# Kernel tuning notes

Measured on AMD Instinct MI355X. Metric: run time of the kernel, lower is better.

## Reference

```python
import jax, jax.numpy as jnp
import numpy as np

DELTA_A, DELTA_R = 0.1, 1.0
ALPHA, BETA, GAMMA = 1.0, 1.0, 0.001


def setup_inputs() -> dict:
    key = jax.random.key(0)
    B, D, H, W, K = 4, 32, 512, 512, 16
    out = jax.random.normal(key, (B, D, H, W), dtype=jnp.float32)
    # 4x4 block partition -> K=16 instance labels, one center per block
    gh, gw = 4, 4
    bh, bw = H // gh, W // gw
    rows = np.arange(H) // bh  # [H]
    cols = np.arange(W) // bw  # [W]
    labels = (rows[:, None] * gw + cols[None, :]).astype(np.int32)  # [H,W]
    target = jnp.asarray(np.broadcast_to(labels, (B, H, W)).copy())
    ctr = np.array([[r * bh + bh // 2, c * bw + bw // 2]
                    for r in range(gh) for c in range(gw)], dtype=np.int32)  # [K,2]
    centers = jnp.asarray(np.broadcast_to(ctr, (B, K, 2)).copy())
    return {"out": out, "target": target, "centers": centers, "batch_size": B}


def _safe_sqrt(x):
    # matches torch.linalg.norm subgradient 0 at 0 (avoids NaN grads)
    pos = x > 0
    return jnp.where(pos, jnp.sqrt(jnp.where(pos, x, 1.0)), 0.0)


def _pairwise_norm(a, b):
    # a [M,D], b [N,D] -> [M,N] euclidean distances via gram trick
    d2 = (jnp.sum(a * a, 1)[:, None] + jnp.sum(b * b, 1)[None, :]
          - 2.0 * a @ b.T)
    return _safe_sqrt(jax.nn.relu(d2))


def _per_image(o, t, c):
    # o [D,H,W], t [H,W] int, c [K,2] int
    D = o.shape[0]
    K = c.shape[0]
    x = o.reshape(D, -1).T                      # [HW, D]
    E = o[:, c[:, 0], c[:, 1]].T                # [K, D] center embeddings
    lab_c = t[c[:, 0], c[:, 1]]                 # [K]
    mask = (t.reshape(-1)[None, :] == lab_c[:, None])  # [K, HW]
    # attraction: hinged distance of every cluster pixel to its center
    norms = _pairwise_norm(E, x)                # [K, HW]
    hinged = jax.nn.relu(norms - DELTA_A) * mask
    cnt = jnp.sum(mask, axis=1)
    denom = jnp.maximum(cnt - 1, 1).astype(o.dtype)
    s_att = jnp.sum(jnp.sum(hinged, axis=1) / denom)
    # repelling: pairwise center distances; diagonal contributes relu(delta_r)
    # per row and the original subtracts delta_r per center -> excluded
    nE = _pairwise_norm(E, E)                   # [K, K]
    s_rep = jnp.sum(jax.nn.relu(DELTA_R - nE)) - K * DELTA_R
    # regularization: norm of each center embedding
    s_reg = jnp.sum(_safe_sqrt(jnp.sum(E * E, axis=1)))
    return s_att, s_rep, s_reg


def reference(out, target, centers, batch_size):
    K = centers.shape[1]
    s_att, s_rep, s_reg = jax.vmap(_per_image)(out, target, centers)  # [B] each
    div_att = jnp.float32(K)
    div_rep = jnp.float32(K * (K - 1))
    div_reg = jnp.float32(K)

    def step(carry, s):
        a, r, g = carry
        sa, sr, sg = s
        return ((a + sa) / div_att, (r + sr) / div_rep, (g + sg) / div_reg), None

    zero = jnp.float32(0.0)
    (att, rep, reg), _ = jax.lax.scan(step, (zero, zero, zero),
                                      (s_att, s_rep, s_reg))
    loss = ALPHA * att + BETA * rep + GAMMA * reg
    return loss, att, rep
```

## Files before the change

### kernel.cpp

```cpp
#include <hip/hip_runtime.h>
#include <hip/hip_bf16.h>

#define B_ 4
#define D_ 32
#define H_ 512
#define W_ 512
#define K_ 16
#define N_ (H_ * W_)
#define NQ_ (N_ / 4)
#define PADK 17
#define EPAD 33

#define WS_SUM  0
#define WS_CNT  64
#define WS_E2   128
#define WS_LAB  192
#define WS_E    264

__global__ __launch_bounds__(64) void setup_kernel(
    const float* __restrict__ outp, const int* __restrict__ target,
    const int* __restrict__ centers, float* __restrict__ ws) {
  const int b = blockIdx.x, k = blockIdx.y;
  const int lane = threadIdx.x;
  const int cy = centers[(b * K_ + k) * 2 + 0];
  const int cx = centers[(b * K_ + k) * 2 + 1];
  float v = 0.0f;
  if (lane < D_) {
    v = outp[(((size_t)b * D_ + lane) * H_ + cy) * W_ + cx];
    ws[WS_E + (b * K_ + k) * D_ + lane] = v;
  }
  float s = v * v;
  for (int off = 32; off > 0; off >>= 1) s += __shfl_xor(s, off, 64);
  if (lane == 0) {
    ws[WS_E2 + b * K_ + k] = s;
    ((int*)ws)[WS_LAB + b * K_ + k] = target[(size_t)b * N_ + cy * W_ + cx];
    ws[WS_SUM + b * K_ + k] = 0.0f;
    ws[WS_CNT + b * K_ + k] = 0.0f;
  }
}

__global__ __launch_bounds__(256) void attract_kernel(
    const float* __restrict__ outp, const int* __restrict__ target,
    float* __restrict__ ws) {
  const int b = blockIdx.y;
  const int tid = threadIdx.x;
  __shared__ float sE[K_ * EPAD];
  __shared__ float se2[K_];
  __shared__ int slab[K_];
  __shared__ float sacc[256 * PADK];
  __shared__ float scnt[256 * PADK];

  for (int i = tid; i < K_ * D_; i += 256) {
    const int k = i >> 5, d = i & 31;
    sE[k * EPAD + d] = ws[WS_E + b * (K_ * D_) + i];
  }
  if (tid < K_) {
    se2[tid] = ws[WS_E2 + b * K_ + tid];
    slab[tid] = ((const int*)ws)[WS_LAB + b * K_ + tid];
  }
#pragma unroll
  for (int k = 0; k < K_; ++k) {
    sacc[tid * PADK + k] = 0.0f;
    scnt[tid * PADK + k] = 0.0f;
  }
  __syncthreads();

  const int q = blockIdx.x * 256 + tid;
  const float4* xb4 = (const float4*)(outp + (size_t)b * D_ * N_);
  const int4 lab4 = ((const int4*)(target + (size_t)b * N_))[q];
  const int labv[4] = {lab4.x, lab4.y, lab4.z, lab4.w};

  int kf[4], nm[4];
#pragma unroll
  for (int j = 0; j < 4; ++j) {
    kf[j] = 0; nm[j] = 0;
#pragma unroll
    for (int k = 0; k < K_; ++k) {
      if (labv[j] == slab[k]) { if (nm[j] == 0) kf[j] = k; nm[j]++; }
    }
  }

  float dot[4] = {0.f, 0.f, 0.f, 0.f};
  float x2[4] = {0.f, 0.f, 0.f, 0.f};
#pragma unroll 8
  for (int d = 0; d < D_; ++d) {
    const float4 x = xb4[(size_t)d * NQ_ + q];
    const float xs[4] = {x.x, x.y, x.z, x.w};
#pragma unroll
    for (int j = 0; j < 4; ++j) {
      const float e = sE[kf[j] * EPAD + d];
      dot[j] = fmaf(xs[j], e, dot[j]);
      x2[j] = fmaf(xs[j], xs[j], x2[j]);
    }
  }

#pragma unroll
  for (int j = 0; j < 4; ++j) {
    if (nm[j] > 0) {
      const int k = kf[j];
      const float d2 = x2[j] + se2[k] - 2.0f * dot[j];
      const float h = fmaxf(sqrtf(fmaxf(d2, 0.0f)) - 0.1f, 0.0f);
      sacc[tid * PADK + k] += h;
      scnt[tid * PADK + k] += 1.0f;
    }
  }

  const bool extra = (nm[0] > 1) | (nm[1] > 1) | (nm[2] > 1) | (nm[3] > 1);
  if (__any(extra)) {
    for (int k = 0; k < K_; ++k) {
      bool need[4]; bool anyn = false;
#pragma unroll
      for (int j = 0; j < 4; ++j) {
        need[j] = (nm[j] > 1) && (labv[j] == slab[k]) && (k != kf[j]);
        anyn |= need[j];
      }
      if (__any(anyn)) {
        float dt[4] = {0.f, 0.f, 0.f, 0.f};
        for (int d = 0; d < D_; ++d) {
          const float4 x = xb4[(size_t)d * NQ_ + q];
          const float xs[4] = {x.x, x.y, x.z, x.w};
#pragma unroll
          for (int j = 0; j < 4; ++j)
            if (need[j]) dt[j] = fmaf(xs[j], sE[k * EPAD + d], dt[j]);
        }
#pragma unroll
        for (int j = 0; j < 4; ++j) {
          if (need[j]) {
            const float d2 = x2[j] + se2[k] - 2.0f * dt[j];
            const float h = fmaxf(sqrtf(fmaxf(d2, 0.0f)) - 0.1f, 0.0f);
            sacc[tid * PADK + k] += h;
            scnt[tid * PADK + k] += 1.0f;
          }
        }
      }
    }
  }
  __syncthreads();

  const int r = tid >> 4, kk = tid & 15;
  float hsum = 0.0f, csum = 0.0f;
#pragma unroll
  for (int j = 0; j < 16; ++j) {
    hsum += sacc[(r * 16 + j) * PADK + kk];
    csum += scnt[(r * 16 + j) * PADK + kk];
  }
  __syncthreads();
  sacc[r * PADK + kk] = hsum;
  scnt[r * PADK + kk] = csum;
  __syncthreads();
  if (tid < K_) {
    float h = 0.0f, c = 0.0f;
#pragma unroll
    for (int rr = 0; rr < 16; ++rr) {
      h += sacc[rr * PADK + tid];
      c += scnt[rr * PADK + tid];
    }
    atomicAdd(&ws[WS_SUM + b * K_ + tid], h);
    atomicAdd(&ws[WS_CNT + b * K_ + tid], c);
  }
}

__global__ __launch_bounds__(256) void final_kernel(const float* __restrict__ ws,
                                                    float* __restrict__ out) {
  __shared__ float sE[B_ * K_ * D_];
  __shared__ float sred[256];
  __shared__ float srep[B_];
  __shared__ float sreg[B_];
  const int tid = threadIdx.x;
  for (int i = tid; i < B_ * K_ * D_; i += 256) sE[i] = ws[WS_E + i];
  __syncthreads();

  const int i = tid >> 4, j = tid & 15;
  for (int b = 0; b < B_; ++b) {
    float dotv = 0.0f;
    for (int d = 0; d < D_; ++d)
      dotv = fmaf(sE[(b * K_ + i) * D_ + d], sE[(b * K_ + j) * D_ + d], dotv);
    const float d2 = ws[WS_E2 + b * K_ + i] + ws[WS_E2 + b * K_ + j] - 2.0f * dotv;
    sred[tid] = fmaxf(1.0f - sqrtf(fmaxf(d2, 0.0f)), 0.0f);
    __syncthreads();
    for (int s = 128; s > 0; s >>= 1) {
      if (tid < s) sred[tid] += sred[tid + s];
      __syncthreads();
    }
    if (tid == 0) srep[b] = sred[0] - (float)K_;
    __syncthreads();
  }

  sred[tid] = (tid < B_ * K_) ? sqrtf(fmaxf(ws[WS_E2 + tid], 0.0f)) : 0.0f;
  __syncthreads();
  if (tid < B_) {
    float s = 0.0f;
    for (int k = 0; k < K_; ++k) s += sred[tid * K_ + k];
    sreg[tid] = s;
  }
  __syncthreads();

  if (tid == 0) {
    float att = 0.0f, rep = 0.0f, reg = 0.0f;
    for (int b = 0; b < B_; ++b) {
      float sa = 0.0f;
      for (int k = 0; k < K_; ++k) {
        const float c = ws[WS_CNT + b * K_ + k];
        sa += ws[WS_SUM + b * K_ + k] / fmaxf(c - 1.0f, 1.0f);
      }
      att = (att + sa) / (float)K_;
      rep = (rep + srep[b]) / (float)(K_ * (K_ - 1));
      reg = (reg + sreg[b]) / (float)K_;
    }
    out[0] = att + rep + 0.001f * reg;
    out[1] = att;
    out[2] = rep;
  }
}

extern "C" void kernel_launch(void* const* d_in, const int* in_sizes, int n_in,
                              void* d_out, int out_size, void* d_ws, size_t ws_size,
                              hipStream_t stream) {
  const float* outp = (const float*)d_in[0];
  const int* target = (const int*)d_in[1];
  const int* centers = (const int*)d_in[2];
  float* ws = (float*)d_ws;
  float* out = (float*)d_out;

  setup_kernel<<<dim3(B_, K_), 64, 0, stream>>>(outp, target, centers, ws);
  attract_kernel<<<dim3(NQ_ / 256, B_), 256, 0, stream>>>(outp, target, ws);
  final_kernel<<<1, 256, 0, stream>>>(ws, out);
}
```

Before: 210.8 us.

## Process two pixels per thread, use LDS atomics and deterministic partial reduction

Each thread now handles two pixels with float2 loads instead of four with float4, which doubles the number of blocks. The large per-thread shared accumulation arrays are replaced by 16-entry LDS atomic accumulators. Global atomics are replaced by per-block partial writes that a new reduce kernel sums. This cuts LDS footprint and raises occupancy, at the cost of LDS atomic contention, narrower loads and one extra kernel launch.

```diff
diff --git a/kernel.cpp b/kernel.cpp
--- a/kernel.cpp
+++ b/kernel.cpp
@@ -7,8 +7,8 @@
 #define W_ 512
 #define K_ 16
 #define N_ (H_ * W_)
-#define NQ_ (N_ / 4)
-#define PADK 17
+#define NH_ (N_ / 2)
+#define NBLK_ 512
 #define EPAD 33
 
 #define WS_SUM  0
@@ -16,6 +16,7 @@
 #define WS_E2   128
 #define WS_LAB  192
 #define WS_E    264
+#define WS_PART 4096
 
 __global__ __launch_bounds__(64) void setup_kernel(
     const float* __restrict__ outp, const int* __restrict__ target,
@@ -34,8 +35,6 @@
   if (lane == 0) {
     ws[WS_E2 + b * K_ + k] = s;
     ((int*)ws)[WS_LAB + b * K_ + k] = target[(size_t)b * N_ + cy * W_ + cx];
-    ws[WS_SUM + b * K_ + k] = 0.0f;
-    ws[WS_CNT + b * K_ + k] = 0.0f;
   }
 }
 
@@ -47,8 +46,8 @@
   __shared__ float sE[K_ * EPAD];
   __shared__ float se2[K_];
   __shared__ int slab[K_];
-  __shared__ float sacc[256 * PADK];
-  __shared__ float scnt[256 * PADK];
+  __shared__ float bs[K_];
+  __shared__ float bc[K_];
 
   for (int i = tid; i < K_ * D_; i += 256) {
     const int k = i >> 5, d = i & 31;
@@ -57,106 +56,101 @@
   if (tid < K_) {
     se2[tid] = ws[WS_E2 + b * K_ + tid];
     slab[tid] = ((const int*)ws)[WS_LAB + b * K_ + tid];
-  }
+    bs[tid] = 0.0f;
+    bc[tid] = 0.0f;
+  }
+  __syncthreads();
+
+  const int g = blockIdx.x * 256 + tid;
+  const float2* xb2 = (const float2*)(outp + (size_t)b * D_ * N_);
+  const int2 lab2 = ((const int2*)(target + (size_t)b * N_))[g];
+
+  int kf0 = 0, kf1 = 0, nm0 = 0, nm1 = 0;
 #pragma unroll
   for (int k = 0; k < K_; ++k) {
-    sacc[tid * PADK + k] = 0.0f;
-    scnt[tid * PADK + k] = 0.0f;
-  }
-  __syncthreads();
-
-  const int q = blockIdx.x * 256 + tid;
-  const float4* xb4 = (const float4*)(outp + (size_t)b * D_ * N_);
-  const int4 lab4 = ((const int4*)(target + (size_t)b * N_))[q];
-  const int labv[4] = {lab4.x, lab4.y, lab4.z, lab4.w};
-
-  int kf[4], nm[4];
-#pragma unroll
-  for (int j = 0; j < 4; ++j) {
-    kf[j] = 0; nm[j] = 0;
-#pragma unroll
-    for (int k = 0; k < K_; ++k) {
-      if (labv[j] == slab[k]) { if (nm[j] == 0) kf[j] = k; nm[j]++; }
-    }
-  }
-
-  float dot[4] = {0.f, 0.f, 0.f, 0.f};
-  float x2[4] = {0.f, 0.f, 0.f, 0.f};
+    const int lk = slab[k];
+    if (lab2.x == lk) { if (nm0 == 0) kf0 = k; nm0++; }
+    if (lab2.y == lk) { if (nm1 == 0) kf1 = k; nm1++; }
+  }
+
+  float dot0 = 0.f, dot1 = 0.f, x20 = 0.f, x21 = 0.f;
 #pragma unroll 8
   for (int d = 0; d < D_; ++d) {
-    const float4 x = xb4[(size_t)d * NQ_ + q];
-    const float xs[4] = {x.x, x.y, x.z, x.w};
-#pragma unroll
-    for (int j = 0; j < 4; ++j) {
-      const float e = sE[kf[j] * EPAD + d];
-      dot[j] = fmaf(xs[j], e, dot[j]);
-      x2[j] = fmaf(xs[j], xs[j], x2[j]);
-    }
-  }
-
-#pragma unroll
-  for (int j = 0; j < 4; ++j) {
-    if (nm[j] > 0) {
-      const int k = kf[j];
-      const float d2 = x2[j] + se2[k] - 2.0f * dot[j];
-      const float h = fmaxf(sqrtf(fmaxf(d2, 0.0f)) - 0.1f, 0.0f);
-      sacc[tid * PADK + k] += h;
-      scnt[tid * PADK + k] += 1.0f;
-    }
-  }
-
-  const bool extra = (nm[0] > 1) | (nm[1] > 1) | (nm[2] > 1) | (nm[3] > 1);
-  if (__any(extra)) {
+    const float2 x = xb2[(size_t)d * NH_ + g];
+    const float e0 = sE[kf0 * EPAD + d];
+    const float e1 = sE[kf1 * EPAD + d];
+    dot0 = fmaf(x.x, e0, dot0);
+    x20  = fmaf(x.x, x.x, x20);
+    dot1 = fmaf(x.y, e1, dot1);
+    x21  = fmaf(x.y, x.y, x21);
+  }
+
+  if (nm0 > 0) {
+    const float d2 = x20 + se2[kf0] - 2.0f * dot0;
+    const float h = fmaxf(sqrtf(fmaxf(d2, 0.0f)) - 0.1f, 0.0f);
+    atomicAdd(&bs[kf0], h);
+    atomicAdd(&bc[kf0], 1.0f);
+  }
+  if (nm1 > 0) {
+    const float d2 = x21 + se2[kf1] - 2.0f * dot1;
+    const float h = fmaxf(sqrtf(fmaxf(d2, 0.0f)) - 0.1f, 0.0f);
+    atomicAdd(&bs[kf1], h);
+    atomicAdd(&bc[kf1], 1.0f);
+  }
+
+  if (__any((nm0 > 1) | (nm1 > 1))) {
     for (int k = 0; k < K_; ++k) {
-      bool need[4]; bool anyn = false;
-#pragma unroll
-      for (int j = 0; j < 4; ++j) {
-        need[j] = (nm[j] > 1) && (labv[j] == slab[k]) && (k != kf[j]);
-        anyn |= need[j];
-      }
-      if (__any(anyn)) {
-        float dt[4] = {0.f, 0.f, 0.f, 0.f};
+      const bool need0 = (nm0 > 1) && (lab2.x == slab[k]) && (k != kf0);
+      const bool need1 = (nm1 > 1) && (lab2.y == slab[k]) && (k != kf1);
+      if (__any(need0 | need1)) {
+        float dt0 = 0.f, dt1 = 0.f;
         for (int d = 0; d < D_; ++d) {
-          const float4 x = xb4[(size_t)d * NQ_ + q];
-          const float xs[4] = {x.x, x.y, x.z, x.w};
-#pragma unroll
-          for (int j = 0; j < 4; ++j)
-            if (need[j]) dt[j] = fmaf(xs[j], sE[k * EPAD + d], dt[j]);
+          const float2 x = xb2[(size_t)d * NH_ + g];
+          const float e = sE[k * EPAD + d];
+          dt0 = fmaf(x.x, e, dt0);
+          dt1 = fmaf(x.y, e, dt1);
         }
-#pragma unroll
-        for (int j = 0; j < 4; ++j) {
-          if (need[j]) {
-            const float d2 = x2[j] + se2[k] - 2.0f * dt[j];
-            const float h = fmaxf(sqrtf(fmaxf(d2, 0.0f)) - 0.1f, 0.0f);
-            sacc[tid * PADK + k] += h;
-            scnt[tid * PADK + k] += 1.0f;
-          }
+        if (need0) {
+          const float d2 = x20 + se2[k] - 2.0f * dt0;
+          atomicAdd(&bs[k], fmaxf(sqrtf(fmaxf(d2, 0.0f)) - 0.1f, 0.0f));
+          atomicAdd(&bc[k], 1.0f);
+        }
+        if (need1) {
+          const float d2 = x21 + se2[k] - 2.0f * dt1;
+          atomicAdd(&bs[k], fmaxf(sqrtf(fmaxf(d2, 0.0f)) - 0.1f, 0.0f));
+          atomicAdd(&bc[k], 1.0f);
         }
       }
     }
   }
   __syncthreads();
 
-  const int r = tid >> 4, kk = tid & 15;
-  float hsum = 0.0f, csum = 0.0f;
-#pragma unroll
-  for (int j = 0; j < 16; ++j) {
-    hsum += sacc[(r * 16 + j) * PADK + kk];
-    csum += scnt[(r * 16 + j) * PADK + kk];
-  }
-  __syncthreads();
-  sacc[r * PADK + kk] = hsum;
-  scnt[r * PADK + kk] = csum;
-  __syncthreads();
-  if (tid < K_) {
-    float h = 0.0f, c = 0.0f;
-#pragma unroll
-    for (int rr = 0; rr < 16; ++rr) {
-      h += sacc[rr * PADK + tid];
-      c += scnt[rr * PADK + tid];
-    }
-    atomicAdd(&ws[WS_SUM + b * K_ + tid], h);
-    atomicAdd(&ws[WS_CNT + b * K_ + tid], c);
+  if (tid < 2 * K_) {
+    float* p = ws + WS_PART + ((size_t)b * NBLK_ + blockIdx.x) * (2 * K_);
+    p[tid] = (tid < K_) ? bs[tid] : bc[tid - K_];
+  }
+}
+
+__global__ __launch_bounds__(256) void reduce_kernel(const float* __restrict__ ws_in,
+                                                     float* __restrict__ ws) {
+  const int b = blockIdx.x >> 4, k = blockIdx.x & 15;
+  const int tid = threadIdx.x;
+  const float* base = ws_in + WS_PART + (size_t)b * NBLK_ * (2 * K_);
+  float s = 0.0f, c = 0.0f;
+  for (int i = tid; i < NBLK_; i += 256) {
+    s += base[i * (2 * K_) + k];
+    c += base[i * (2 * K_) + K_ + k];
+  }
+  for (int off = 32; off > 0; off >>= 1) {
+    s += __shfl_xor(s, off, 64);
+    c += __shfl_xor(c, off, 64);
+  }
+  __shared__ float rs[4], rc[4];
+  if ((tid & 63) == 0) { rs[tid >> 6] = s; rc[tid >> 6] = c; }
+  __syncthreads();
+  if (tid == 0) {
+    ws[WS_SUM + b * K_ + k] = rs[0] + rs[1] + rs[2] + rs[3];
+    ws[WS_CNT + b * K_ + k] = rc[0] + rc[1] + rc[2] + rc[3];
   }
 }
 
@@ -223,6 +217,7 @@
   float* out = (float*)d_out;
 
   setup_kernel<<<dim3(B_, K_), 64, 0, stream>>>(outp, target, centers, ws);
-  attract_kernel<<<dim3(NQ_ / 256, B_), 256, 0, stream>>>(outp, target, ws);
+  attract_kernel<<<dim3(NBLK_, B_), 256, 0, stream>>>(outp, target, ws);
+  reduce_kernel<<<dim3(B_ * K_), 256, 0, stream>>>(ws, ws);
   final_kernel<<<1, 256, 0, stream>>>(ws, out);
 }
```

New measurement: 220.0 us. +4.4%, slower.

## Replace per-thread LDS accumulators with shared atomics and two-stage partial reduction

Applied to the files above, without the earlier changes.

Drops the large 256x17 per-thread shared-memory accumulator arrays in favour of 16-entry shared atomics, with a fast path that issues one atomic when all four pixels belong to the same cluster. Per-block partial sums go to workspace and a new reduce kernel combines them, replacing global atomics and removing the need to zero them in setup. Loads of the embedding and label streams use nontemporal hints and the D loop is fully unrolled. This cuts LDS footprint, which should raise occupancy for the bandwidth-bound stream, at the cost of an extra kernel launch and possible shared-atomic contention.

```diff
diff --git a/kernel.cpp b/kernel.cpp
--- a/kernel.cpp
+++ b/kernel.cpp
@@ -8,7 +8,7 @@
 #define K_ 16
 #define N_ (H_ * W_)
 #define NQ_ (N_ / 4)
-#define PADK 17
+#define NBLK_ 256
 #define EPAD 33
 
 #define WS_SUM  0
@@ -16,6 +16,17 @@
 #define WS_E2   128
 #define WS_LAB  192
 #define WS_E    264
+#define WS_PART 4096
+
+typedef float vfloat4 __attribute__((ext_vector_type(4)));
+typedef int vint4 __attribute__((ext_vector_type(4)));
+
+__device__ inline vfloat4 nt_load_f4(const float* p) {
+  return __builtin_nontemporal_load((const vfloat4*)p);
+}
+__device__ inline vint4 nt_load_i4(const int* p) {
+  return __builtin_nontemporal_load((const vint4*)p);
+}
 
 __global__ __launch_bounds__(64) void setup_kernel(
     const float* __restrict__ outp, const int* __restrict__ target,
@@ -34,8 +45,6 @@
   if (lane == 0) {
     ws[WS_E2 + b * K_ + k] = s;
     ((int*)ws)[WS_LAB + b * K_ + k] = target[(size_t)b * N_ + cy * W_ + cx];
-    ws[WS_SUM + b * K_ + k] = 0.0f;
-    ws[WS_CNT + b * K_ + k] = 0.0f;
   }
 }
 
@@ -47,44 +56,47 @@
   __shared__ float sE[K_ * EPAD];
   __shared__ float se2[K_];
   __shared__ int slab[K_];
-  __shared__ float sacc[256 * PADK];
-  __shared__ float scnt[256 * PADK];
-
-  for (int i = tid; i < K_ * D_; i += 256) {
-    const int k = i >> 5, d = i & 31;
-    sE[k * EPAD + d] = ws[WS_E + b * (K_ * D_) + i];
+  __shared__ float bs[K_];
+  __shared__ float bc[K_];
+
+  if (tid < 128) {
+    const vfloat4 v = *(const vfloat4*)(ws + WS_E + b * (K_ * D_) + tid * 4);
+    const int k = tid >> 3, d = (tid & 7) * 4;
+    sE[k * EPAD + d + 0] = v.x;
+    sE[k * EPAD + d + 1] = v.y;
+    sE[k * EPAD + d + 2] = v.z;
+    sE[k * EPAD + d + 3] = v.w;
   }
   if (tid < K_) {
     se2[tid] = ws[WS_E2 + b * K_ + tid];
     slab[tid] = ((const int*)ws)[WS_LAB + b * K_ + tid];
-  }
+    bs[tid] = 0.0f;
+    bc[tid] = 0.0f;
+  }
+  __syncthreads();
+
+  const int q = blockIdx.x * 256 + tid;
+  const float* xb = outp + (size_t)b * D_ * N_;
+  const vint4 lab4 = nt_load_i4(target + (size_t)b * N_ + 4 * q);
+  const int labv[4] = {lab4.x, lab4.y, lab4.z, lab4.w};
+
+  int kf[4], nm[4];
+#pragma unroll
+  for (int j = 0; j < 4; ++j) { kf[j] = 0; nm[j] = 0; }
 #pragma unroll
   for (int k = 0; k < K_; ++k) {
-    sacc[tid * PADK + k] = 0.0f;
-    scnt[tid * PADK + k] = 0.0f;
-  }
-  __syncthreads();
-
-  const int q = blockIdx.x * 256 + tid;
-  const float4* xb4 = (const float4*)(outp + (size_t)b * D_ * N_);
-  const int4 lab4 = ((const int4*)(target + (size_t)b * N_))[q];
-  const int labv[4] = {lab4.x, lab4.y, lab4.z, lab4.w};
-
-  int kf[4], nm[4];
-#pragma unroll
-  for (int j = 0; j < 4; ++j) {
-    kf[j] = 0; nm[j] = 0;
-#pragma unroll
-    for (int k = 0; k < K_; ++k) {
-      if (labv[j] == slab[k]) { if (nm[j] == 0) kf[j] = k; nm[j]++; }
+    const int lk = slab[k];
+#pragma unroll
+    for (int j = 0; j < 4; ++j) {
+      if (labv[j] == lk) { if (nm[j] == 0) kf[j] = k; nm[j]++; }
     }
   }
 
   float dot[4] = {0.f, 0.f, 0.f, 0.f};
   float x2[4] = {0.f, 0.f, 0.f, 0.f};
-#pragma unroll 8
+#pragma unroll
   for (int d = 0; d < D_; ++d) {
-    const float4 x = xb4[(size_t)d * NQ_ + q];
+    const vfloat4 x = nt_load_f4(xb + (size_t)d * N_ + 4 * q);
     const float xs[4] = {x.x, x.y, x.z, x.w};
 #pragma unroll
     for (int j = 0; j < 4; ++j) {
@@ -94,14 +106,27 @@
     }
   }
 
+  float hv[4];
 #pragma unroll
   for (int j = 0; j < 4; ++j) {
-    if (nm[j] > 0) {
-      const int k = kf[j];
-      const float d2 = x2[j] + se2[k] - 2.0f * dot[j];
-      const float h = fmaxf(sqrtf(fmaxf(d2, 0.0f)) - 0.1f, 0.0f);
-      sacc[tid * PADK + k] += h;
-      scnt[tid * PADK + k] += 1.0f;
+    const float d2 = x2[j] + se2[kf[j]] - 2.0f * dot[j];
+    const float h = fmaxf(sqrtf(fmaxf(d2, 0.0f)) - 0.1f, 0.0f);
+    hv[j] = (nm[j] > 0) ? h : 0.0f;
+  }
+  const bool same = (kf[0] == kf[1]) & (kf[1] == kf[2]) & (kf[2] == kf[3]);
+  if (same) {
+    const float cs = (float)((nm[0] > 0) + (nm[1] > 0) + (nm[2] > 0) + (nm[3] > 0));
+    if (cs > 0.0f) {
+      atomicAdd(&bs[kf[0]], hv[0] + hv[1] + hv[2] + hv[3]);
+      atomicAdd(&bc[kf[0]], cs);
+    }
+  } else {
+#pragma unroll
+    for (int j = 0; j < 4; ++j) {
+      if (nm[j] > 0) {
+        atomicAdd(&bs[kf[j]], hv[j]);
+        atomicAdd(&bc[kf[j]], 1.0f);
+      }
     }
   }
 
@@ -117,19 +142,19 @@
       if (__any(anyn)) {
         float dt[4] = {0.f, 0.f, 0.f, 0.f};
         for (int d = 0; d < D_; ++d) {
-          const float4 x = xb4[(size_t)d * NQ_ + q];
-          const float xs[4] = {x.x, x.y, x.z, x.w};
-#pragma unroll
-          for (int j = 0; j < 4; ++j)
-            if (need[j]) dt[j] = fmaf(xs[j], sE[k * EPAD + d], dt[j]);
+          const vfloat4 x = nt_load_f4(xb + (size_t)d * N_ + 4 * q);
+          const float e = sE[k * EPAD + d];
+          dt[0] = fmaf(x.x, e, dt[0]);
+          dt[1] = fmaf(x.y, e, dt[1]);
+          dt[2] = fmaf(x.z, e, dt[2]);
+          dt[3] = fmaf(x.w, e, dt[3]);
         }
 #pragma unroll
         for (int j = 0; j < 4; ++j) {
           if (need[j]) {
             const float d2 = x2[j] + se2[k] - 2.0f * dt[j];
-            const float h = fmaxf(sqrtf(fmaxf(d2, 0.0f)) - 0.1f, 0.0f);
-            sacc[tid * PADK + k] += h;
-            scnt[tid * PADK + k] += 1.0f;
+            atomicAdd(&bs[k], fmaxf(sqrtf(fmaxf(d2, 0.0f)) - 0.1f, 0.0f));
+            atomicAdd(&bc[k], 1.0f);
           }
         }
       }
@@ -137,26 +162,32 @@
   }
   __syncthreads();
 
-  const int r = tid >> 4, kk = tid & 15;
-  float hsum = 0.0f, csum = 0.0f;
-#pragma unroll
-  for (int j = 0; j < 16; ++j) {
-    hsum += sacc[(r * 16 + j) * PADK + kk];
-    csum += scnt[(r * 16 + j) * PADK + kk];
-  }
-  __syncthreads();
-  sacc[r * PADK + kk] = hsum;
-  scnt[r * PADK + kk] = csum;
-  __syncthreads();
-  if (tid < K_) {
-    float h = 0.0f, c = 0.0f;
-#pragma unroll
-    for (int rr = 0; rr < 16; ++rr) {
-      h += sacc[rr * PADK + tid];
-      c += scnt[rr * PADK + tid];
-    }
-    atomicAdd(&ws[WS_SUM + b * K_ + tid], h);
-    atomicAdd(&ws[WS_CNT + b * K_ + tid], c);
+  if (tid < 2 * K_) {
+    float* p = ws + WS_PART + ((size_t)b * NBLK_ + blockIdx.x) * (2 * K_);
+    p[tid] = (tid < K_) ? bs[tid] : bc[tid - K_];
+  }
+}
+
+__global__ __launch_bounds__(256) void reduce_kernel(const float* __restrict__ ws_in,
+                                                     float* __restrict__ ws) {
+  const int b = blockIdx.x >> 4, k = blockIdx.x & 15;
+  const int tid = threadIdx.x;
+  const float* base = ws_in + WS_PART + (size_t)b * NBLK_ * (2 * K_);
+  float s = 0.0f, c = 0.0f;
+  for (int i = tid; i < NBLK_; i += 256) {
+    s += base[i * (2 * K_) + k];
+    c += base[i * (2 * K_) + K_ + k];
+  }
+  for (int off = 32; off > 0; off >>= 1) {
+    s += __shfl_xor(s, off, 64);
+    c += __shfl_xor(c, off, 64);
+  }
+  __shared__ float rs[4], rc[4];
+  if ((tid & 63) == 0) { rs[tid >> 6] = s; rc[tid >> 6] = c; }
+  __syncthreads();
+  if (tid == 0) {
+    ws[WS_SUM + b * K_ + k] = rs[0] + rs[1] + rs[2] + rs[3];
+    ws[WS_CNT + b * K_ + k] = rc[0] + rc[1] + rc[2] + rc[3];
   }
 }
 
@@ -166,6 +197,7 @@
   __shared__ float sred[256];
   __shared__ float srep[B_];
   __shared__ float sreg[B_];
+  __shared__ float ssa[B_];
   const int tid = threadIdx.x;
   for (int i = tid; i < B_ * K_ * D_; i += 256) sE[i] = ws[WS_E + i];
   __syncthreads();
@@ -173,6 +205,7 @@
   const int i = tid >> 4, j = tid & 15;
   for (int b = 0; b < B_; ++b) {
     float dotv = 0.0f;
+#pragma unroll 8
     for (int d = 0; d < D_; ++d)
       dotv = fmaf(sE[(b * K_ + i) * D_ + d], sE[(b * K_ + j) * D_ + d], dotv);
     const float d2 = ws[WS_E2 + b * K_ + i] + ws[WS_E2 + b * K_ + j] - 2.0f * dotv;
@@ -193,17 +226,19 @@
     for (int k = 0; k < K_; ++k) s += sred[tid * K_ + k];
     sreg[tid] = s;
   }
+
+  if (tid < B_ * K_) {
+    const float c = ws[WS_CNT + tid];
+    float v = ws[WS_SUM + tid] / fmaxf(c - 1.0f, 1.0f);
+    for (int off = 1; off < K_; off <<= 1) v += __shfl_xor(v, off, 64);
+    if ((tid & 15) == 0) ssa[tid >> 4] = v;
+  }
   __syncthreads();
 
   if (tid == 0) {
     float att = 0.0f, rep = 0.0f, reg = 0.0f;
     for (int b = 0; b < B_; ++b) {
-      float sa = 0.0f;
-      for (int k = 0; k < K_; ++k) {
-        const float c = ws[WS_CNT + b * K_ + k];
-        sa += ws[WS_SUM + b * K_ + k] / fmaxf(c - 1.0f, 1.0f);
-      }
-      att = (att + sa) / (float)K_;
+      att = (att + ssa[b]) / (float)K_;
       rep = (rep + srep[b]) / (float)(K_ * (K_ - 1));
       reg = (reg + sreg[b]) / (float)K_;
     }
@@ -223,6 +258,7 @@
   float* out = (float*)d_out;
 
   setup_kernel<<<dim3(B_, K_), 64, 0, stream>>>(outp, target, centers, ws);
-  attract_kernel<<<dim3(NQ_ / 256, B_), 256, 0, stream>>>(outp, target, ws);
+  attract_kernel<<<dim3(NBLK_, B_), 256, 0, stream>>>(outp, target, ws);
+  reduce_kernel<<<dim3(B_ * K_), 256, 0, stream>>>(ws, ws);
   final_kernel<<<1, 256, 0, stream>>>(ws, out);
 }
```

After: 200.2 us. 1.05x faster.
